# Performance work log

Measured on AMD Instinct MI355X. Metric: run time of the kernel, lower is better.

The kernel has to match this reference:

```python
import jax, jax.numpy as jnp
import numpy as np


def _forward(x, conv_w, conv_b, lin_w, lin_b, W_in, conv1d_w, conv1d_b, W_x, W_dt, b_dt, A_log, Dp, W_out, We, be, Wa, ba, Wq, bq):
    B, _, H, Wd = x.shape
    E = conv_w.shape[0]
    # conv stem: Conv2d(k=3, pad=1) -> flatten(2) -> Linear(H*W -> img_size)
    z = jax.lax.conv_general_dilated(x, conv_w, (1, 1), [(1, 1), (1, 1)],
                                     dimension_numbers=('NCHW', 'OIHW', 'NCHW'))
    z = z + conv_b[None, :, None, None]
    z = z.reshape(B, E, H * Wd)                              # [B,E,HW]
    z = jnp.einsum('ben,mn->bem', z, lin_w) + lin_b          # [B,E,L]
    u = z.transpose(2, 0, 1)                                 # [L,B,E]: Mamba sees batch=L, seq=B
    # ---- Mamba block (mamba_ssm reference math) ----
    di = W_in.shape[0] // 2
    xz = u @ W_in.T                                          # [L,seq,2*di]
    xm, zg = xz[..., :di], xz[..., di:]
    K = conv1d_w.shape[-1]
    xc = jax.lax.conv_general_dilated(xm.transpose(0, 2, 1), conv1d_w, (1,), [(K - 1, 0)],
                                      dimension_numbers=('NCH', 'OIH', 'NCH'),
                                      feature_group_count=di)  # causal depthwise conv
    xs = jax.nn.silu((xc + conv1d_b[None, :, None]).transpose(0, 2, 1))  # [L,seq,di]
    dbl = xs @ W_x.T                                         # [L,seq,dt_rank+2S]
    dt_rank = W_dt.shape[1]
    S = A_log.shape[1]
    delta = jax.nn.softplus(dbl[..., :dt_rank] @ W_dt.T + b_dt)          # [L,seq,di]
    Bm = dbl[..., dt_rank:dt_rank + S]                       # [L,seq,S]
    Cm = dbl[..., dt_rank + S:]                              # [L,seq,S]
    A = -jnp.exp(A_log)                                      # [di,S]

    def step(h, t):
        d_t, b_t, c_t, x_t = t                               # [L,di],[L,S],[L,S],[L,di]
        h = jnp.exp(d_t[:, :, None] * A) * h + (d_t * x_t)[:, :, None] * b_t[:, None, :]
        return h, jnp.einsum('lds,ls->ld', h, c_t)

    h0 = jnp.zeros((u.shape[0], di, S), xs.dtype)
    _, ys = jax.lax.scan(step, h0, (delta.transpose(1, 0, 2), Bm.transpose(1, 0, 2),
                                    Cm.transpose(1, 0, 2), xs.transpose(1, 0, 2)))
    y = (ys.transpose(1, 0, 2) + xs * Dp) * jax.nn.silu(zg)  # [L,seq,di]
    out = y @ W_out.T                                        # [L,seq,E]
    feat = out[-1]                                           # [B,E] (last 'mamba batch' row)
    return feat @ We.T + be, feat @ Wa.T + ba, feat @ Wq.T + bq


def setup_inputs() -> dict:
    key = jax.random.key(0)
    ks = jax.random.split(key, 16)
    B, C, IMG, E, S, K = 512, 1, 32, 128, 256, 4
    di, dt_rank = 2 * E, 8
    sc = 0.02
    return {
        'x': jax.random.normal(ks[0], (B, C, IMG, IMG), jnp.float32),
        'conv_w': sc * jax.random.normal(ks[1], (E, C, 3, 3), jnp.float32),
        'conv_b': jnp.zeros((E,), jnp.float32),
        'lin_w': sc * jax.random.normal(ks[2], (IMG, IMG * IMG), jnp.float32),
        'lin_b': jnp.zeros((IMG,), jnp.float32),
        'W_in': sc * jax.random.normal(ks[3], (2 * di, E), jnp.float32),
        'conv1d_w': sc * jax.random.normal(ks[4], (di, 1, K), jnp.float32),
        'conv1d_b': jnp.zeros((di,), jnp.float32),
        'W_x': sc * jax.random.normal(ks[5], (dt_rank + 2 * S, di), jnp.float32),
        'W_dt': sc * jax.random.normal(ks[6], (di, dt_rank), jnp.float32),
        'b_dt': 0.1 * jax.random.normal(ks[7], (di,), jnp.float32),
        'A_log': jnp.log(jnp.broadcast_to(jnp.arange(1, S + 1, dtype=jnp.float32), (di, S))),
        'Dp': jnp.ones((di,), jnp.float32),
        'W_out': sc * jax.random.normal(ks[8], (E, di), jnp.float32),
        'We': sc * jax.random.normal(ks[9], (1, E), jnp.float32),
        'be': jnp.zeros((1,), jnp.float32),
        'Wa': sc * jax.random.normal(ks[10], (3, E), jnp.float32),
        'ba': jnp.zeros((3,), jnp.float32),
        'Wq': sc * jax.random.normal(ks[11], (4, E), jnp.float32),
        'bq': jnp.zeros((4,), jnp.float32),
    }


def reference(x, conv_w, conv_b, lin_w, lin_b, W_in, conv1d_w, conv1d_b, W_x, W_dt, b_dt, A_log, Dp, W_out, We, be, Wa, ba, Wq, bq):
    return _forward(x, conv_w, conv_b, lin_w, lin_b, W_in, conv1d_w, conv1d_b, W_x,
                    W_dt, b_dt, A_log, Dp, W_out, We, be, Wa, ba, Wq, bq)
```

## Files before the change

kernel.cpp:

```cpp
#include <hip/hip_runtime.h>
#include <math.h>

#define BATCH 512
#define E     128
#define DI    256
#define S     256
#define DTR   8
#define KCONV 4
#define JWX   520
#define NC    32
#define TCV   (BATCH / NC)

__device__ __forceinline__ float silu_f(float v) {
    return v / (1.0f + __expf(-v));
}

__global__ __launch_bounds__(256) void kA_pre(
    const float* __restrict__ x, const float* __restrict__ conv_w,
    const float* __restrict__ conv_b, const float* __restrict__ lin_w,
    const float* __restrict__ lin_b, const float* __restrict__ W_in,
    float* __restrict__ xm, float* __restrict__ zg)
{
    const int tid = threadIdx.x;
    const int bb = blockIdx.x * 2;
    __shared__ float lw[1024];
    __shared__ float red[10][4];
    __shared__ float Tsh[10];
    __shared__ float u0[E];
    __shared__ float u1[E];

    const float4 lv = ((const float4*)(lin_w + 31 * 1024))[tid];
    ((float4*)lw)[tid] = lv;
    __syncthreads();

    const int wv = tid >> 6, ln = tid & 63;

    for (int r = 0; r < 2; r++) {
        const int b = bb + r;

        float acc[10];
#pragma unroll
        for (int k = 0; k < 10; k++) acc[k] = 0.0f;

        const float4 xv = ((const float4*)(x + (size_t)b * 1024))[tid];
        const int p0 = tid * 4;
        const int h = p0 >> 5, w0 = p0 & 31;
        const float xa[4] = {xv.x, xv.y, xv.z, xv.w};
#pragma unroll
        for (int k = 0; k < 4; k++) {
            const float xval = xa[k];
            const int w = w0 + k;
#pragma unroll
            for (int i = 0; i < 3; i++) {
                const int hh = h - (i - 1);
                if (hh < 0 || hh > 31) continue;
#pragma unroll
                for (int j = 0; j < 3; j++) {
                    const int ww = w - (j - 1);
                    if (ww < 0 || ww > 31) continue;
                    acc[i * 3 + j] += xval * lw[hh * 32 + ww];
                }
            }
        }
        acc[9] = lv.x + lv.y + lv.z + lv.w;

        float R0, q4;
        {
            float q0, q1, q2, q3;
            {
                const bool b0 = (ln & 1);
                float s_, r_;
                s_ = b0 ? acc[0] : acc[1]; r_ = __shfl_xor(s_, 1, 64);
                q0 = (b0 ? acc[1] : acc[0]) + r_;
                s_ = b0 ? acc[2] : acc[3]; r_ = __shfl_xor(s_, 1, 64);
                q1 = (b0 ? acc[3] : acc[2]) + r_;
                s_ = b0 ? acc[4] : acc[5]; r_ = __shfl_xor(s_, 1, 64);
                q2 = (b0 ? acc[5] : acc[4]) + r_;
                s_ = b0 ? acc[6] : acc[7]; r_ = __shfl_xor(s_, 1, 64);
                q3 = (b0 ? acc[7] : acc[6]) + r_;
                s_ = b0 ? acc[8] : acc[9]; r_ = __shfl_xor(s_, 1, 64);
                q4 = (b0 ? acc[9] : acc[8]) + r_;
            }
            {
                const bool b1 = (ln & 2);
                float s_, r_;
                s_ = b1 ? q0 : q1; r_ = __shfl_xor(s_, 2, 64);
                q0 = (b1 ? q1 : q0) + r_;
                s_ = b1 ? q2 : q3; r_ = __shfl_xor(s_, 2, 64);
                q1 = (b1 ? q3 : q2) + r_;
                q4 += __shfl_xor(q4, 2, 64);
            }
            {
                const bool b2 = (ln & 4);
                const float s_ = b2 ? q0 : q1;
                const float r_ = __shfl_xor(s_, 4, 64);
                R0 = (b2 ? q1 : q0) + r_;
                q4 += __shfl_xor(q4, 4, 64);
            }
            R0 += __shfl_xor(R0, 8, 64);
            R0 += __shfl_xor(R0, 16, 64);
            R0 += __shfl_xor(R0, 32, 64);
            q4 += __shfl_xor(q4, 8, 64);
            q4 += __shfl_xor(q4, 16, 64);
            q4 += __shfl_xor(q4, 32, 64);
        }
        if (ln < 8) red[ln][wv] = R0;
        if (ln < 2) red[8 + ln][wv] = q4;
        __syncthreads();
        if (tid < 10) Tsh[tid] = red[tid][0] + red[tid][1] + red[tid][2] + red[tid][3];
        __syncthreads();

        if (tid < E) {
            const int e = tid;
            float v = lin_b[31] + conv_b[e] * Tsh[9];
#pragma unroll
            for (int k = 0; k < 9; k++) v += conv_w[e * 9 + k] * Tsh[k];
            if (r == 0) u0[e] = v; else u1[e] = v;
        }
        __syncthreads();
    }

    {
        const float4* w0p = (const float4*)(W_in + (size_t)tid * E);
        const float4* w1p = (const float4*)(W_in + (size_t)(tid + 256) * E);
        float a00 = 0.0f, a01 = 0.0f;
#pragma unroll 8
        for (int e4 = 0; e4 < E / 4; e4++) {
            const float4 w = w0p[e4];
            a00 += u0[4*e4]*w.x + u0[4*e4+1]*w.y + u0[4*e4+2]*w.z + u0[4*e4+3]*w.w;
            a01 += u1[4*e4]*w.x + u1[4*e4+1]*w.y + u1[4*e4+2]*w.z + u1[4*e4+3]*w.w;
        }
        float a10 = 0.0f, a11 = 0.0f;
#pragma unroll 8
        for (int e4 = 0; e4 < E / 4; e4++) {
            const float4 w = w1p[e4];
            a10 += u0[4*e4]*w.x + u0[4*e4+1]*w.y + u0[4*e4+2]*w.z + u0[4*e4+3]*w.w;
            a11 += u1[4*e4]*w.x + u1[4*e4+1]*w.y + u1[4*e4+2]*w.z + u1[4*e4+3]*w.w;
        }
        xm[(bb + 0) * DI + tid] = a00;
        xm[(bb + 1) * DI + tid] = a01;
        zg[(bb + 0) * DI + tid] = a10;
        zg[(bb + 1) * DI + tid] = a11;
    }
}

__global__ __launch_bounds__(256) void k2b_conv_wx(
    const float* __restrict__ xm, const float* __restrict__ c1w,
    const float* __restrict__ conv1d_b, const float* __restrict__ W_x,
    const float* __restrict__ W_dt, const float* __restrict__ b_dt,
    float* __restrict__ xs_g, float* __restrict__ delta_g,
    float* __restrict__ Bm, float* __restrict__ Cm)
{
    const int bb = blockIdx.x * 4;
    const int gy = blockIdx.y;
    const int tid = threadIdx.x;
    __shared__ float xs_sh[4][DI];
    __shared__ float dtin[4][8];

    for (int idx = tid; idx < 4 * DI; idx += 256) {
        const int r = idx >> 8, c = idx & 255;
        const int b = bb + r;
        const float4 wc = ((const float4*)c1w)[c];
        float a = conv1d_b[c];
        if (b >= 3) a += xm[(b - 3) * DI + c] * wc.x;
        if (b >= 2) a += xm[(b - 2) * DI + c] * wc.y;
        if (b >= 1) a += xm[(b - 1) * DI + c] * wc.z;
        a += xm[b * DI + c] * wc.w;
        const float s = silu_f(a);
        xs_sh[r][c] = s;
        if (gy == 0) xs_g[b * DI + c] = s;
    }
    __syncthreads();

    for (int jl = tid; jl < 260; jl += 256) {
        const int jj = gy * 260 + jl;
        const float4* wr = (const float4*)(W_x + (size_t)jj * DI);
        const float4* x0 = (const float4*)xs_sh[0];
        const float4* x1 = (const float4*)xs_sh[1];
        const float4* x2 = (const float4*)xs_sh[2];
        const float4* x3 = (const float4*)xs_sh[3];
        float a0 = 0.0f, a1 = 0.0f, a2 = 0.0f, a3 = 0.0f;
#pragma unroll 8
        for (int c4 = 0; c4 < 64; c4++) {
            const float4 w  = wr[c4];
            const float4 v0 = x0[c4];
            const float4 v1 = x1[c4];
            const float4 v2 = x2[c4];
            const float4 v3 = x3[c4];
            a0 += v0.x*w.x; a0 += v0.y*w.y; a0 += v0.z*w.z; a0 += v0.w*w.w;
            a1 += v1.x*w.x; a1 += v1.y*w.y; a1 += v1.z*w.z; a1 += v1.w*w.w;
            a2 += v2.x*w.x; a2 += v2.y*w.y; a2 += v2.z*w.z; a2 += v2.w*w.w;
            a3 += v3.x*w.x; a3 += v3.y*w.y; a3 += v3.z*w.z; a3 += v3.w*w.w;
        }
        const float av[4] = {a0, a1, a2, a3};
        if (jj < DTR) {
#pragma unroll
            for (int r = 0; r < 4; r++) dtin[r][jj] = av[r];
        } else if (jj < DTR + S) {
#pragma unroll
            for (int r = 0; r < 4; r++) Bm[(bb + r) * S + (jj - DTR)] = av[r];
        } else {
#pragma unroll
            for (int r = 0; r < 4; r++) Cm[(bb + r) * S + (jj - DTR - S)] = av[r];
        }
    }
    __syncthreads();

    if (gy == 0) {
        const int d = tid;
        const float bd = b_dt[d];
        const float4 wd0 = ((const float4*)(W_dt + d * DTR))[0];
        const float4 wd1 = ((const float4*)(W_dt + d * DTR))[1];
#pragma unroll
        for (int r2 = 0; r2 < 4; r2++) {
            float a = bd
                + dtin[r2][0]*wd0.x + dtin[r2][1]*wd0.y + dtin[r2][2]*wd0.z + dtin[r2][3]*wd0.w
                + dtin[r2][4]*wd1.x + dtin[r2][5]*wd1.y + dtin[r2][6]*wd1.z + dtin[r2][7]*wd1.w;
            const float sp = (a > 20.0f) ? a : log1pf(__expf(a));
            delta_g[(bb + r2) * DI + d] = sp;
        }
    }
}

__global__ __launch_bounds__(256) void k3u_up(
    const float* __restrict__ A_log, const float* __restrict__ delta,
    const float* __restrict__ xs, const float* __restrict__ Bm,
    float* __restrict__ hloc, float* __restrict__ Dchunk)
{
    const int tid = threadIdx.x;
    const int wv = tid >> 6, ln = tid & 63;
    const int d = blockIdx.x * 4 + wv;
    const int c = blockIdx.y;
    const int s0 = ln * 4;
    const int t0 = c * TCV;

    const float4 al = *(const float4*)(A_log + d * S + s0);
    float4 A;
    A.x = -__expf(al.x); A.y = -__expf(al.y);
    A.z = -__expf(al.z); A.w = -__expf(al.w);

    float4 h = make_float4(0.f, 0.f, 0.f, 0.f);
    float cd = 0.0f;
    for (int tb = 0; tb < TCV; tb += 8) {
#pragma unroll
        for (int i = 0; i < 8; i++) {
            const int tt = t0 + tb + i;
            const float dd = delta[tt * DI + d];
            cd += dd;
            const float u = dd * xs[tt * DI + d];
            const float4 B = *(const float4*)(Bm + tt * S + s0);
            h.x = __expf(dd * A.x) * h.x + u * B.x;
            h.y = __expf(dd * A.y) * h.y + u * B.y;
            h.z = __expf(dd * A.z) * h.z + u * B.z;
            h.w = __expf(dd * A.w) * h.w + u * B.w;
        }
    }
    *(float4*)(hloc + ((size_t)(c * DI + d)) * S + s0) = h;
    if (ln == 0) Dchunk[c * DI + d] = cd;
}

__global__ __launch_bounds__(256) void k3d_down(
    const float* __restrict__ A_log, const float* __restrict__ delta,
    const float* __restrict__ xs, const float* __restrict__ Bm,
    const float* __restrict__ Cm, const float* __restrict__ hloc,
    const float* __restrict__ Dchunk, float* __restrict__ y)
{
    const int tid = threadIdx.x;
    const int wv = tid >> 6, ln = tid & 63;
    const int d = blockIdx.x * 4 + wv;
    const int c = (NC - 1) - blockIdx.y;
    const int s0 = ln * 4;
    const int t0 = c * TCV;

    const float4 al = *(const float4*)(A_log + d * S + s0);
    float4 A;
    A.x = -__expf(al.x); A.y = -__expf(al.y);
    A.z = -__expf(al.z); A.w = -__expf(al.w);

    float4 h = make_float4(0.f, 0.f, 0.f, 0.f);
    for (int cp = 1; cp <= c; cp++) {
        const float4 hl = *(const float4*)(hloc + ((size_t)((cp - 1) * DI + d)) * S + s0);
        const float Dc = Dchunk[(cp - 1) * DI + d];
        h.x = hl.x + __expf(A.x * Dc) * h.x;
        h.y = hl.y + __expf(A.y * Dc) * h.y;
        h.z = hl.z + __expf(A.z * Dc) * h.z;
        h.w = hl.w + __expf(A.w * Dc) * h.w;
    }

    float pr[8];
    for (int tb = 0; tb < TCV; tb += 8) {
#pragma unroll
        for (int i = 0; i < 8; i++) {
            const int tt = t0 + tb + i;
            const float dd = delta[tt * DI + d];
            const float u = dd * xs[tt * DI + d];
            const float4 B = *(const float4*)(Bm + tt * S + s0);
            const float4 C = *(const float4*)(Cm + tt * S + s0);
            h.x = __expf(dd * A.x) * h.x + u * B.x;
            h.y = __expf(dd * A.y) * h.y + u * B.y;
            h.z = __expf(dd * A.z) * h.z + u * B.z;
            h.w = __expf(dd * A.w) * h.w + u * B.w;
            pr[i] = h.x * C.x + h.y * C.y + h.z * C.z + h.w * C.w;
        }

        float q0, q1, q2, q3;
        {
            const bool b0 = (ln & 1);
            float s_, r_;
            s_ = b0 ? pr[0] : pr[1]; r_ = __shfl_xor(s_, 1, 64);
            q0 = (b0 ? pr[1] : pr[0]) + r_;
            s_ = b0 ? pr[2] : pr[3]; r_ = __shfl_xor(s_, 1, 64);
            q1 = (b0 ? pr[3] : pr[2]) + r_;
            s_ = b0 ? pr[4] : pr[5]; r_ = __shfl_xor(s_, 1, 64);
            q2 = (b0 ? pr[5] : pr[4]) + r_;
            s_ = b0 ? pr[6] : pr[7]; r_ = __shfl_xor(s_, 1, 64);
            q3 = (b0 ? pr[7] : pr[6]) + r_;
        }
        {
            const bool b1 = (ln & 2);
            float s_, r_;
            s_ = b1 ? q0 : q1; r_ = __shfl_xor(s_, 2, 64);
            q0 = (b1 ? q1 : q0) + r_;
            s_ = b1 ? q2 : q3; r_ = __shfl_xor(s_, 2, 64);
            q1 = (b1 ? q3 : q2) + r_;
        }
        {
            const bool b2 = (ln & 4);
            const float s_ = b2 ? q0 : q1;
            const float r_ = __shfl_xor(s_, 4, 64);
            q0 = (b2 ? q1 : q0) + r_;
        }
        q0 += __shfl_xor(q0, 8, 64);
        q0 += __shfl_xor(q0, 16, 64);
        q0 += __shfl_xor(q0, 32, 64);
        if (ln < 8) y[(t0 + tb + ln) * DI + d] = q0;
    }
}

__global__ __launch_bounds__(256) void k4_heads(
    const float* __restrict__ y, const float* __restrict__ xs,
    const float* __restrict__ Dp, const float* __restrict__ zg,
    const float* __restrict__ W_out,
    const float* __restrict__ We, const float* __restrict__ be,
    const float* __restrict__ Wa, const float* __restrict__ ba,
    const float* __restrict__ Wq, const float* __restrict__ bq,
    float* __restrict__ out)
{
    const int bb = blockIdx.x * 2;
    const int tid = threadIdx.x;
    __shared__ float yf[2][DI];
    __shared__ float feat[2][E];

    for (int idx = tid; idx < 2 * DI; idx += 256) {
        const int r = idx >> 8, c = idx & 255;
        const int b = bb + r;
        const float z = zg[b * DI + c];
        yf[r][c] = (y[b * DI + c] + xs[b * DI + c] * Dp[c]) * silu_f(z);
    }
    __syncthreads();

    {
        const int r = tid >> 7, e = tid & 127;
        const float4* wr = (const float4*)(W_out + (size_t)e * DI);
        const float4* yv = (const float4*)yf[r];
        float a = 0.0f;
#pragma unroll 8
        for (int d4 = 0; d4 < 64; d4++) {
            const float4 w = wr[d4];
            const float4 v = yv[d4];
            a += v.x * w.x; a += v.y * w.y; a += v.z * w.z; a += v.w * w.w;
        }
        feat[r][e] = a;
    }
    __syncthreads();

    if (tid < 16) {
        const int r = tid >> 3, hd = tid & 7;
        const int b = bb + r;
        const float* wrow;
        float bias;
        int dst;
        if (hd == 0)      { wrow = We;                 bias = be[0];      dst = b; }
        else if (hd < 4)  { wrow = Wa + (hd - 1) * E;  bias = ba[hd - 1]; dst = 512 + b * 3 + (hd - 1); }
        else              { wrow = Wq + (hd - 4) * E;  bias = bq[hd - 4]; dst = 2048 + b * 4 + (hd - 4); }
        float a = bias;
#pragma unroll 4
        for (int e = 0; e < E; e++) a += feat[r][e] * wrow[e];
        out[dst] = a;
    }
}

extern "C" void kernel_launch(void* const* d_in, const int* in_sizes, int n_in,
                              void* d_out, int out_size, void* d_ws, size_t ws_size,
                              hipStream_t stream)
{
    const float* x        = (const float*)d_in[0];
    const float* conv_w   = (const float*)d_in[1];
    const float* conv_b   = (const float*)d_in[2];
    const float* lin_w    = (const float*)d_in[3];
    const float* lin_b    = (const float*)d_in[4];
    const float* W_in     = (const float*)d_in[5];
    const float* conv1d_w = (const float*)d_in[6];
    const float* conv1d_b = (const float*)d_in[7];
    const float* W_x      = (const float*)d_in[8];
    const float* W_dt     = (const float*)d_in[9];
    const float* b_dt     = (const float*)d_in[10];
    const float* A_log    = (const float*)d_in[11];
    const float* Dp       = (const float*)d_in[12];
    const float* W_out    = (const float*)d_in[13];
    const float* We       = (const float*)d_in[14];
    const float* be       = (const float*)d_in[15];
    const float* Wa       = (const float*)d_in[16];
    const float* ba       = (const float*)d_in[17];
    const float* Wq       = (const float*)d_in[18];
    const float* bq       = (const float*)d_in[19];
    float* out = (float*)d_out;

    float* ws = (float*)d_ws;
    float* xm     = ws;
    float* zg     = xm     + 512 * 256;
    float* xs     = zg     + 512 * 256;
    float* delta  = xs     + 512 * 256;
    float* Bm     = delta  + 512 * 256;
    float* Cm     = Bm     + 512 * 256;
    float* y      = Cm     + 512 * 256;
    float* hloc   = y      + 512 * 256;
    float* Dchunk = hloc   + (size_t)NC * DI * S;

    kA_pre<<<256, 256, 0, stream>>>(x, conv_w, conv_b, lin_w, lin_b, W_in,
                                    xm, zg);
    k2b_conv_wx<<<dim3(128, 2), 256, 0, stream>>>(xm, conv1d_w, conv1d_b, W_x,
                                                  W_dt, b_dt, xs, delta, Bm, Cm);
    k3u_up<<<dim3(64, NC), 256, 0, stream>>>(A_log, delta, xs, Bm, hloc, Dchunk);
    k3d_down<<<dim3(64, NC), 256, 0, stream>>>(A_log, delta, xs, Bm, Cm,
                                               hloc, Dchunk, y);
    k4_heads<<<256, 256, 0, stream>>>(y, xs, Dp, zg, W_out, We, be, Wa, ba, Wq, bq, out);
}
```

Baseline: 174.2 us.

## Fuse conv stem, in-projection, causal conv and x-projection into one kernel

Merges the stem/in-projection kernel and the depthwise-conv/W_x kernel into a single kernel. Each block handles four sequence positions and recomputes the three preceding positions' xm (a 3-position halo), so xm never goes to global memory and one launch and a dependency point are removed. The cost is redundant stem and W_in work for the halo (7 rows computed per 4 kept). The grid also shrinks to 128 blocks, each with the full 520-row W_x loop, where before the W_x work was split across two blocks per group.

```diff
diff --git a/kernel.cpp b/kernel.cpp
--- a/kernel.cpp
+++ b/kernel.cpp
@@ -15,28 +15,36 @@
     return v / (1.0f + __expf(-v));
 }
 
-__global__ __launch_bounds__(256) void kA_pre(
+__global__ __launch_bounds__(256) void kfront(
     const float* __restrict__ x, const float* __restrict__ conv_w,
     const float* __restrict__ conv_b, const float* __restrict__ lin_w,
     const float* __restrict__ lin_b, const float* __restrict__ W_in,
-    float* __restrict__ xm, float* __restrict__ zg)
+    const float* __restrict__ c1w, const float* __restrict__ conv1d_b,
+    const float* __restrict__ W_x, const float* __restrict__ W_dt,
+    const float* __restrict__ b_dt,
+    float* __restrict__ zg, float* __restrict__ xs_g,
+    float* __restrict__ delta_g, float* __restrict__ Bm,
+    float* __restrict__ Cm)
 {
     const int tid = threadIdx.x;
-    const int bb = blockIdx.x * 2;
+    const int g = blockIdx.x, bb = g * 4;
+    const int wv = tid >> 6, ln = tid & 63;
+
     __shared__ float lw[1024];
     __shared__ float red[10][4];
     __shared__ float Tsh[10];
-    __shared__ float u0[E];
-    __shared__ float u1[E];
+    __shared__ float u[7][E];
+    __shared__ float xml[7][DI];
+    __shared__ float xs_sh[4][DI];
+    __shared__ float dtin[4][8];
 
     const float4 lv = ((const float4*)(lin_w + 31 * 1024))[tid];
     ((float4*)lw)[tid] = lv;
     __syncthreads();
 
-    const int wv = tid >> 6, ln = tid & 63;
-
-    for (int r = 0; r < 2; r++) {
-        const int b = bb + r;
+    for (int i = 0; i < 7; i++) {
+        const int b = bb - 3 + i;
+        if (b < 0) continue;
 
         float acc[10];
 #pragma unroll
@@ -51,14 +59,14 @@
             const float xval = xa[k];
             const int w = w0 + k;
 #pragma unroll
-            for (int i = 0; i < 3; i++) {
-                const int hh = h - (i - 1);
+            for (int ii = 0; ii < 3; ii++) {
+                const int hh = h - (ii - 1);
                 if (hh < 0 || hh > 31) continue;
 #pragma unroll
                 for (int j = 0; j < 3; j++) {
                     const int ww = w - (j - 1);
                     if (ww < 0 || ww > 31) continue;
-                    acc[i * 3 + j] += xval * lw[hh * 32 + ww];
+                    acc[ii * 3 + j] += xval * lw[hh * 32 + ww];
                 }
             }
         }
@@ -115,7 +123,7 @@
             float v = lin_b[31] + conv_b[e] * Tsh[9];
 #pragma unroll
             for (int k = 0; k < 9; k++) v += conv_w[e * 9 + k] * Tsh[k];
-            if (r == 0) u0[e] = v; else u1[e] = v;
+            u[i][e] = v;
         }
         __syncthreads();
     }
@@ -123,57 +131,49 @@
     {
         const float4* w0p = (const float4*)(W_in + (size_t)tid * E);
         const float4* w1p = (const float4*)(W_in + (size_t)(tid + 256) * E);
-        float a00 = 0.0f, a01 = 0.0f;
-#pragma unroll 8
+        float ax[7] = {0.f, 0.f, 0.f, 0.f, 0.f, 0.f, 0.f};
+        float az[4] = {0.f, 0.f, 0.f, 0.f};
+#pragma unroll 4
         for (int e4 = 0; e4 < E / 4; e4++) {
-            const float4 w = w0p[e4];
-            a00 += u0[4*e4]*w.x + u0[4*e4+1]*w.y + u0[4*e4+2]*w.z + u0[4*e4+3]*w.w;
-            a01 += u1[4*e4]*w.x + u1[4*e4+1]*w.y + u1[4*e4+2]*w.z + u1[4*e4+3]*w.w;
-        }
-        float a10 = 0.0f, a11 = 0.0f;
-#pragma unroll 8
-        for (int e4 = 0; e4 < E / 4; e4++) {
-            const float4 w = w1p[e4];
-            a10 += u0[4*e4]*w.x + u0[4*e4+1]*w.y + u0[4*e4+2]*w.z + u0[4*e4+3]*w.w;
-            a11 += u1[4*e4]*w.x + u1[4*e4+1]*w.y + u1[4*e4+2]*w.z + u1[4*e4+3]*w.w;
-        }
-        xm[(bb + 0) * DI + tid] = a00;
-        xm[(bb + 1) * DI + tid] = a01;
-        zg[(bb + 0) * DI + tid] = a10;
-        zg[(bb + 1) * DI + tid] = a11;
-    }
-}
-
-__global__ __launch_bounds__(256) void k2b_conv_wx(
-    const float* __restrict__ xm, const float* __restrict__ c1w,
-    const float* __restrict__ conv1d_b, const float* __restrict__ W_x,
-    const float* __restrict__ W_dt, const float* __restrict__ b_dt,
-    float* __restrict__ xs_g, float* __restrict__ delta_g,
-    float* __restrict__ Bm, float* __restrict__ Cm)
-{
-    const int bb = blockIdx.x * 4;
-    const int gy = blockIdx.y;
-    const int tid = threadIdx.x;
-    __shared__ float xs_sh[4][DI];
-    __shared__ float dtin[4][8];
-
-    for (int idx = tid; idx < 4 * DI; idx += 256) {
-        const int r = idx >> 8, c = idx & 255;
-        const int b = bb + r;
-        const float4 wc = ((const float4*)c1w)[c];
-        float a = conv1d_b[c];
-        if (b >= 3) a += xm[(b - 3) * DI + c] * wc.x;
-        if (b >= 2) a += xm[(b - 2) * DI + c] * wc.y;
-        if (b >= 1) a += xm[(b - 1) * DI + c] * wc.z;
-        a += xm[b * DI + c] * wc.w;
-        const float s = silu_f(a);
-        xs_sh[r][c] = s;
-        if (gy == 0) xs_g[b * DI + c] = s;
-    }
-    __syncthreads();
-
-    for (int jl = tid; jl < 260; jl += 256) {
-        const int jj = gy * 260 + jl;
+            const float4 w  = w0p[e4];
+            const float4 w2 = w1p[e4];
+#pragma unroll
+            for (int i = 0; i < 7; i++) {
+                ax[i] += u[i][4*e4]*w.x + u[i][4*e4+1]*w.y
+                       + u[i][4*e4+2]*w.z + u[i][4*e4+3]*w.w;
+            }
+#pragma unroll
+            for (int r = 0; r < 4; r++) {
+                az[r] += u[3 + r][4*e4]*w2.x + u[3 + r][4*e4+1]*w2.y
+                       + u[3 + r][4*e4+2]*w2.z + u[3 + r][4*e4+3]*w2.w;
+            }
+        }
+#pragma unroll
+        for (int i = 0; i < 7; i++) xml[i][tid] = ax[i];
+#pragma unroll
+        for (int r = 0; r < 4; r++) zg[(bb + r) * DI + tid] = az[r];
+    }
+    __syncthreads();
+
+    {
+        const float4 wc = ((const float4*)c1w)[tid];
+        const float cb = conv1d_b[tid];
+#pragma unroll
+        for (int r = 0; r < 4; r++) {
+            const int b = bb + r;
+            float a = cb;
+            if (b >= 3) a += xml[r + 0][tid] * wc.x;
+            if (b >= 2) a += xml[r + 1][tid] * wc.y;
+            if (b >= 1) a += xml[r + 2][tid] * wc.z;
+            a += xml[r + 3][tid] * wc.w;
+            const float s = silu_f(a);
+            xs_sh[r][tid] = s;
+            xs_g[b * DI + tid] = s;
+        }
+    }
+    __syncthreads();
+
+    for (int jj = tid; jj < JWX; jj += 256) {
         const float4* wr = (const float4*)(W_x + (size_t)jj * DI);
         const float4* x0 = (const float4*)xs_sh[0];
         const float4* x1 = (const float4*)xs_sh[1];
@@ -206,7 +206,7 @@
     }
     __syncthreads();
 
-    if (gy == 0) {
+    {
         const int d = tid;
         const float bd = b_dt[d];
         const float4 wd0 = ((const float4*)(W_dt + d * DTR))[0];
@@ -417,8 +417,7 @@
     float* out = (float*)d_out;
 
     float* ws = (float*)d_ws;
-    float* xm     = ws;
-    float* zg     = xm     + 512 * 256;
+    float* zg     = ws;
     float* xs     = zg     + 512 * 256;
     float* delta  = xs     + 512 * 256;
     float* Bm     = delta  + 512 * 256;
@@ -427,10 +426,9 @@
     float* hloc   = y      + 512 * 256;
     float* Dchunk = hloc   + (size_t)NC * DI * S;
 
-    kA_pre<<<256, 256, 0, stream>>>(x, conv_w, conv_b, lin_w, lin_b, W_in,
-                                    xm, zg);
-    k2b_conv_wx<<<dim3(128, 2), 256, 0, stream>>>(xm, conv1d_w, conv1d_b, W_x,
-                                                  W_dt, b_dt, xs, delta, Bm, Cm);
+    kfront<<<128, 256, 0, stream>>>(x, conv_w, conv_b, lin_w, lin_b, W_in,
+                                    conv1d_w, conv1d_b, W_x, W_dt, b_dt,
+                                    zg, xs, delta, Bm, Cm);
     k3u_up<<<dim3(64, NC), 256, 0, stream>>>(A_log, delta, xs, Bm, hloc, Dchunk);
     k3d_down<<<dim3(64, NC), 256, 0, stream>>>(A_log, delta, xs, Bm, Cm,
                                                hloc, Dchunk, y);
```

After: 189.4 us. +8.7%, slower.
